# Kernel optimization log

Hardware: AMD Instinct MI355X
Metric: run time of the kernel (lower is better)

Reference implementation:

```python
import jax, jax.numpy as jnp
import numpy as np

B, N_PER, K = 8, 4096, 16          # graphs, nodes per graph, knn neighbors
D_IN, D_H, D_OUT = 32, 64, 128     # feature_nn: 35->64->64, global_nn: 64->128
N = B * N_PER


def setup_inputs() -> dict:
    key = jax.random.key(0)
    ks = jax.random.split(key, 8)
    sc = lambda fan: 1.0 / np.sqrt(fan)
    x = jax.random.normal(ks[0], (N, D_IN), jnp.float32)
    pos = jax.random.normal(ks[1], (N, 3), jnp.float32)
    batch = jnp.repeat(jnp.arange(B, dtype=jnp.int32), N_PER)
    fW1 = jax.random.normal(ks[2], (D_IN + 3, D_H), jnp.float32) * sc(D_IN + 3)
    fb1 = jnp.zeros((D_H,), jnp.float32)
    fW2 = jax.random.normal(ks[3], (D_H, D_H), jnp.float32) * sc(D_H)
    fb2 = jnp.zeros((D_H,), jnp.float32)
    gW = jax.random.normal(ks[4], (D_H, D_OUT), jnp.float32) * sc(D_H)
    gb = jnp.zeros((D_OUT,), jnp.float32)
    return {"x": x, "pos": pos, "batch": batch,
            "fW1": fW1, "fb1": fb1, "fW2": fW2, "fb2": fb2,
            "gW": gW, "gb": gb}


def reference(x, pos, batch, fW1, fb1, fW2, fb2, gW, gb):
    # ---- knn(pos, pos, k, batch, batch): per-graph k nearest (self included) ----
    posb = pos.reshape(B, N_PER, 3)
    sq = jnp.sum(posb * posb, axis=-1)                      # [B, Nper]
    dist = sq[:, :, None] + sq[:, None, :] - 2.0 * jnp.einsum('bnd,bmd->bnm', posb, posb)
    _, nbr = jax.lax.top_k(-dist, K)                        # [B, Nper, K] local neighbor idx
    offs = (jnp.arange(B, dtype=nbr.dtype) * N_PER)[:, None, None]
    col = (nbr + offs).reshape(-1)                          # edge_index[1]: neighbor (x) idx
    row = jnp.repeat(jnp.arange(N, dtype=col.dtype), K)     # edge_index[0]: query (y) idx

    # ---- PointConv: msg = feature_nn(cat[x_j, pos_j - pos_i]), max-aggregate at i ----
    # PyG flow source_to_target: j = edge_index[0] = row (query), i = edge_index[1] = col.
    msg = jnp.concatenate([x[row], pos[row] - pos[col]], axis=1)  # [E, 35]
    h = jax.nn.relu(msg @ fW1 + fb1)
    h = jax.nn.relu(h @ fW2 + fb2)                          # [E, 64]
    agg = jax.ops.segment_max(h, col, num_segments=N)       # max aggregation
    agg = jnp.where(jnp.isfinite(agg), agg, 0.0)            # PyG fills empty segments with 0
    out = jax.nn.relu(agg @ gW + gb)                        # global_nn
    return (out, pos, batch)
```

## Files before the change

kernel.cpp:

```cpp
#include <hip/hip_runtime.h>
#include <hip/hip_bf16.h>

#define N_PER    4096
#define KNBR     16
#define NTOT     32768
#define D_IN     32
#define D_H      64
#define D_OUT    128
#define E_TOT    (NTOT * KNBR)

#define OUT1_OFF (NTOT * D_OUT)
#define OUT2_OFF (NTOT * D_OUT + NTOT*3)

#define KNN_INF 3.4e38f

typedef __attribute__((ext_vector_type(8))) short bf16x8;
typedef __attribute__((ext_vector_type(4))) float f32x4;

__device__ float          g_posf[NTOT * 3];
__device__ float          g_scf[NTOT];
__device__ float4         g_pos4[NTOT];
__device__ int            g_nbr[E_TOT];
__device__ unsigned short g_base1h[NTOT * D_H];
__device__ uint4          g_Bfrag[2 * 4 * 64];
__device__ float          g_Wd[3 * D_H];
__device__ float          g_fb2v[D_H];
__device__ int            g_cnt[NTOT];
__device__ int            g_bsum[NTOT / 256];
__device__ int            g_offs[NTOT + 1];
__device__ int            g_cursor[NTOT];
__device__ int            g_inlist[E_TOT];
__device__ float          g_agg[NTOT * D_H];

__device__ __forceinline__ float ldf(const void* p, int i, int bf) {
    if (bf) return __uint_as_float(((unsigned)((const unsigned short*)p)[i]) << 16);
    return ((const float*)p)[i];
}
__device__ __forceinline__ unsigned bf16rne(float f) {
    unsigned u = __float_as_uint(f);
    return (u + 0x7FFFu + ((u >> 16) & 1u)) >> 16;
}
__device__ __forceinline__ void stf(void* p, int i, float v, int bf) {
    if (bf) ((unsigned short*)p)[i] = (unsigned short)bf16rne(v);
    else    ((float*)p)[i] = v;
}
__device__ __forceinline__ float b2f(unsigned short h) {
    return __uint_as_float(((unsigned)h) << 16);
}
__device__ __forceinline__ int wave_probe(const void* x) {
    unsigned wv = ((const unsigned*)x)[threadIdx.x & 63];
    unsigned e = (wv >> 7) & 0xFFu;
    unsigned long long mk = __ballot(e >= 110u && e <= 140u);
    return (__popcll(mk) >= 32) ? 1 : 0;
}

__global__ __launch_bounds__(256) void prep_kernel(const void* __restrict__ x,
                                                   const void* __restrict__ pos,
                                                   const void* __restrict__ fW1,
                                                   const void* __restrict__ fb1,
                                                   const void* __restrict__ fW2,
                                                   const void* __restrict__ fb2) {
    const int bf = wave_probe(x);
    const int b = blockIdx.x;
    if (b < 1024) {
        const int i0 = b * 256 + threadIdx.x;
        const int stride = 1024 * 256;
        for (int i = i0; i < NTOT * 3; i += stride) g_posf[i] = ldf(pos, i, bf);
        {
#pragma clang fp contract(off)
            for (int i = i0; i < NTOT; i += stride) {
                float a = ldf(pos, i * 3 + 0, bf);
                float c2 = ldf(pos, i * 3 + 1, bf);
                float c3 = ldf(pos, i * 3 + 2, bf);
                float sc = a * a + c2 * c2 + c3 * c3;
                g_scf[i] = sc;
                g_pos4[i] = make_float4(-2.0f * a, -2.0f * c2, -2.0f * c3, sc);
                g_cnt[i] = 0;
            }
        }
        for (int i = i0; i < NTOT * D_H; i += stride) g_agg[i] = 0.0f;
    } else if (b < 2048) {
        int lane = threadIdx.x & 63, wid = threadIdx.x >> 6;
        int n0 = (b - 1024) * 32 + wid * 8;
        float wcol[D_IN];
#pragma unroll
        for (int k = 0; k < D_IN; k++) wcol[k] = ldf(fW1, k * D_H + lane, bf);
        float bb = ldf(fb1, lane, bf);
        if (bf) {
            const unsigned short* xp = (const unsigned short*)x;
            for (int r = 0; r < 8; r++) {
                int n = n0 + r;
                const uint4* xr = (const uint4*)(xp + (size_t)n * D_IN);
                float acc = bb;
#pragma unroll
                for (int q4 = 0; q4 < 4; q4++) {
                    uint4 w4 = xr[q4];
                    unsigned ww[4] = {w4.x, w4.y, w4.z, w4.w};
#pragma unroll
                    for (int p = 0; p < 4; p++) {
                        int k = q4 * 8 + p * 2;
                        acc += __uint_as_float(ww[p] << 16) * wcol[k];
                        acc += __uint_as_float(ww[p] & 0xFFFF0000u) * wcol[k + 1];
                    }
                }
                g_base1h[(size_t)n * D_H + lane] = (unsigned short)bf16rne(acc);
            }
        } else {
            const float* xp = (const float*)x;
            for (int r = 0; r < 8; r++) {
                int n = n0 + r;
                const float4* xr = (const float4*)(xp + (size_t)n * D_IN);
                float acc = bb;
#pragma unroll
                for (int q4 = 0; q4 < 8; q4++) {
                    float4 w4 = xr[q4];
                    int k = q4 * 4;
                    acc += w4.x * wcol[k] + w4.y * wcol[k + 1] + w4.z * wcol[k + 2] + w4.w * wcol[k + 3];
                }
                g_base1h[(size_t)n * D_H + lane] = (unsigned short)bf16rne(acc);
            }
        }
    } else {
        for (int t = threadIdx.x; t < 3 * D_H; t += 256) g_Wd[t] = ldf(fW1, D_IN * D_H + t, bf);
        if (threadIdx.x < D_H) g_fb2v[threadIdx.x] = ldf(fb2, threadIdx.x, bf);
        for (int idx = threadIdx.x; idx < 512; idx += 256) {
            int lane = idx & 63, nt = (idx >> 6) & 3, ks = idx >> 8;
            int n = nt * 16 + (lane & 15);
            int k0 = ks * 32 + ((lane >> 4) << 3);
            unsigned wds[4];
#pragma unroll
            for (int jp = 0; jp < 4; jp++) {
                unsigned lo = bf16rne(ldf(fW2, (k0 + 2 * jp) * D_H + n, bf));
                unsigned hi = bf16rne(ldf(fW2, (k0 + 2 * jp + 1) * D_H + n, bf));
                wds[jp] = lo | (hi << 16);
            }
            g_Bfrag[idx] = make_uint4(wds[0], wds[1], wds[2], wds[3]);
        }
    }
}

__global__ __launch_bounds__(512) void knn_kernel() {
#pragma clang fp contract(off)
    __shared__ float4 s_c4[2048];
    __shared__ int s_i[8][8][64];
    const int lane = threadIdx.x & 63;
    const int wid  = threadIdx.x >> 6;
    const int qbase = blockIdx.x * 64 + wid * 8;
    const int cbase = (qbase >> 12) << 12;
    const float* cp  = g_posf + cbase * 3;
    const float* csc = g_scf + cbase;

    float qx[8], qy[8], qz[8], qs[8];
#pragma unroll
    for (int r = 0; r < 8; r++) {
        qx[r] = g_posf[(qbase + r) * 3 + 0];
        qy[r] = g_posf[(qbase + r) * 3 + 1];
        qz[r] = g_posf[(qbase + r) * 3 + 2];
        qs[r] = g_scf[qbase + r];
    }

    float m[8];
#pragma unroll
    for (int r = 0; r < 8; r++) m[r] = KNN_INF;
    for (int ch = 0; ch < 2; ch++) {
        __syncthreads();
        const float4* gp = g_pos4 + cbase + ch * 2048;
        for (int i = threadIdx.x; i < 2048; i += 512) s_c4[i] = gp[i];
        __syncthreads();
#pragma unroll 4
        for (int c = 0; c < 32; c++) {
            float4 v4 = s_c4[c * 64 + lane];
#pragma unroll
            for (int r = 0; r < 8; r++) {
                float d = fmaf(v4.z, qz[r], fmaf(v4.y, qy[r], fmaf(v4.x, qx[r], v4.w)));
                m[r] = fminf(m[r], d);
            }
        }
    }

    float T[8];
#pragma unroll
    for (int r = 0; r < 8; r++) {
        float v = m[r];
#pragma unroll
        for (int k = 2; k <= 64; k <<= 1) {
#pragma unroll
            for (int j2 = k >> 1; j2 >= 1; j2 >>= 1) {
                float pv = __shfl_xor(v, j2);
                bool keepMin = (((lane & j2) == 0) == ((lane & k) == 0));
                bool tp = ((pv < v) == keepMin);
                v = tp ? pv : v;
            }
        }
        T[r] = __shfl(v, 15) + 1e-3f;
    }

    int cnt[8];
#pragma unroll
    for (int r = 0; r < 8; r++) cnt[r] = 0;
    for (int ch = 0; ch < 2; ch++) {
        __syncthreads();
        const float4* gp = g_pos4 + cbase + ch * 2048;
        for (int i = threadIdx.x; i < 2048; i += 512) s_c4[i] = gp[i];
        __syncthreads();
        for (int c = 0; c < 32; c++) {
            int jj = c * 64 + lane;
            float4 v4 = s_c4[jj];
#pragma unroll
            for (int r = 0; r < 8; r++) {
                float d = fmaf(v4.z, qz[r], fmaf(v4.y, qy[r], fmaf(v4.x, qx[r], v4.w)));
                bool p = (d <= T[r]);
                unsigned long long mk = __ballot(p);
                if (mk) {
                    int pre = (int)__popcll(mk & ((1ull << lane) - 1ull));
                    int slot = cnt[r] + pre;
                    if (p && slot < 64) s_i[wid][r][slot] = cbase + ch * 2048 + jj;
                    cnt[r] += (int)__popcll(mk);
                }
            }
        }
    }

#pragma unroll
    for (int r = 0; r < 8; r++) {
        int q = qbase + r;
        if (cnt[r] <= 64) {
            int S = cnt[r];
            int idx = (lane < S) ? s_i[wid][r][lane] : 0x7FFFFFFF;
            float d = KNN_INF;
            if (lane < S) {
                float px = g_posf[idx * 3], py = g_posf[idx * 3 + 1], pz = g_posf[idx * 3 + 2];
                float sc = g_scf[idx];
                float dot = px * qx[r] + py * qy[r] + pz * qz[r];
                d = (qs[r] + sc) - 2.0f * dot;
            }
#pragma unroll
            for (int k = 2; k <= 64; k <<= 1) {
#pragma unroll
                for (int j2 = k >> 1; j2 >= 1; j2 >>= 1) {
                    float pd = __shfl_xor(d, j2);
                    int   pi = __shfl_xor(idx, j2);
                    bool keepMin = (((lane & j2) == 0) == ((lane & k) == 0));
                    bool lt = (pd < d) || (pd == d && pi < idx);
                    bool tp = (lt == keepMin);
                    d   = tp ? pd : d;
                    idx = tp ? pi : idx;
                }
            }
            if (lane < 16) {
                g_nbr[q * KNBR + lane] = idx;
                atomicAdd(&g_cnt[idx & (NTOT - 1)], 1);
            }
        } else {
            float lastd = -KNN_INF; int lasti = -1;
            for (int t = 0; t < 16; t++) {
                float bd = KNN_INF; int bi = 0x7FFFFFFF;
                for (int c = 0; c < 64; c++) {
                    int jj = c * 64 + lane;
                    float px = cp[jj * 3], py = cp[jj * 3 + 1], pz = cp[jj * 3 + 2];
                    float sc = csc[jj];
                    float dot = px * qx[r] + py * qy[r] + pz * qz[r];
                    float dd = (qs[r] + sc) - 2.0f * dot;
                    int gj = cbase + jj;
                    bool after  = (dd > lastd) || (dd == lastd && gj > lasti);
                    bool better = (dd < bd) || (dd == bd && gj < bi);
                    if (after && better) { bd = dd; bi = gj; }
                }
#pragma unroll
                for (int s2 = 1; s2 < 64; s2 <<= 1) {
                    float od = __shfl_xor(bd, s2);
                    int   oi = __shfl_xor(bi, s2);
                    if (od < bd || (od == bd && oi < bi)) { bd = od; bi = oi; }
                }
                if (lane == 0) {
                    g_nbr[q * KNBR + t] = bi;
                    atomicAdd(&g_cnt[bi & (NTOT - 1)], 1);
                }
                lastd = bd; lasti = bi;
            }
        }
    }
}

__global__ __launch_bounds__(256) void scanA_kernel() {
    __shared__ int red[4];
    int t = threadIdx.x, lane = t & 63, w = t >> 6;
    int v = g_cnt[blockIdx.x * 256 + t];
    int s = v;
#pragma unroll
    for (int off = 1; off < 64; off <<= 1) s += __shfl_xor(s, off);
    if (lane == 0) red[w] = s;
    __syncthreads();
    if (t == 0) g_bsum[blockIdx.x] = red[0] + red[1] + red[2] + red[3];
}

__global__ __launch_bounds__(256) void scanC_kernel() {
    __shared__ int sred[4];
    __shared__ int wsum[4];
    int t = threadIdx.x, lane = t & 63, w = t >> 6;
    int contrib = (t < 128 && t < blockIdx.x) ? g_bsum[t] : 0;
    int rs = contrib;
#pragma unroll
    for (int off = 1; off < 64; off <<= 1) rs += __shfl_xor(rs, off);
    if (lane == 0) sred[w] = rs;
    __syncthreads();
    int base = sred[0] + sred[1] + sred[2] + sred[3];

    int i = blockIdx.x * 256 + t;
    int v = g_cnt[i];
    int inc = v;
#pragma unroll
    for (int off = 1; off < 64; off <<= 1) {
        int u = __shfl_up(inc, off);
        if (lane >= off) inc += u;
    }
    if (lane == 63) wsum[w] = inc;
    __syncthreads();
    int wbase = 0;
    for (int k = 0; k < w; k++) wbase += wsum[k];
    int excl = base + wbase + inc - v;
    g_offs[i] = excl;
    g_cursor[i] = excl;
    if (i == NTOT - 1) g_offs[NTOT] = E_TOT;
}

__global__ void scatter_kernel() {
    int e = blockIdx.x * 256 + threadIdx.x;
    int c = g_nbr[e] & (NTOT - 1);
    int slot = atomicAdd(&g_cursor[c], 1);
    g_inlist[slot & (E_TOT - 1)] = e;
}

__global__ __launch_bounds__(256) void edge_kernel() {
    __shared__ unsigned short sA[256 * 72];
    __shared__ int scol[256];
    const int t    = threadIdx.x;
    const int lane = t & 63;
    const int w    = t >> 6;
    const int slot0 = blockIdx.x * 256;

    {
        int e = g_inlist[slot0 + t];
        int n = (e >> 4) & (NTOT - 1);
        int j = g_nbr[e] & (NTOT - 1);
        scol[t] = j;
        float dx = g_posf[n * 3 + 0] - g_posf[j * 3 + 0];
        float dy = g_posf[n * 3 + 1] - g_posf[j * 3 + 1];
        float dz = g_posf[n * 3 + 2] - g_posf[j * 3 + 2];
        const unsigned short* b1 = g_base1h + (size_t)n * D_H;
#pragma unroll
        for (int d0 = 0; d0 < D_H; d0 += 8) {
            uint4 p = *(const uint4*)(b1 + d0);
            unsigned pw[4] = {p.x, p.y, p.z, p.w};
            unsigned qw[4];
#pragma unroll
            for (int jp = 0; jp < 4; jp++) {
                int d = d0 + 2 * jp;
                float v0 = __uint_as_float(pw[jp] << 16)
                         + dx * g_Wd[d]     + dy * g_Wd[64 + d]     + dz * g_Wd[128 + d];
                float v1 = __uint_as_float(pw[jp] & 0xFFFF0000u)
                         + dx * g_Wd[d + 1] + dy * g_Wd[64 + d + 1] + dz * g_Wd[128 + d + 1];
                v0 = fmaxf(v0, 0.f); v1 = fmaxf(v1, 0.f);
                qw[jp] = bf16rne(v0) | (bf16rne(v1) << 16);
            }
            *(uint4*)(&sA[t * 72 + d0]) = make_uint4(qw[0], qw[1], qw[2], qw[3]);
        }
    }
    __syncthreads();

    f32x4 acc[4][4];
#pragma unroll
    for (int a = 0; a < 4; a++)
#pragma unroll
        for (int b = 0; b < 4; b++) acc[a][b] = (f32x4){0.f, 0.f, 0.f, 0.f};

    const int quad = lane >> 4;
    const int l15  = lane & 15;
#pragma unroll
    for (int ks = 0; ks < 2; ks++) {
        bf16x8 bfrag[4];
#pragma unroll
        for (int nt = 0; nt < 4; nt++)
            bfrag[nt] = ((const bf16x8*)g_Bfrag)[ks * 256 + nt * 64 + lane];
#pragma unroll
        for (int mt = 0; mt < 4; mt++) {
            int row = w * 64 + mt * 16 + l15;
            bf16x8 afrag = *(const bf16x8*)(&sA[row * 72 + ks * 32 + quad * 8]);
#pragma unroll
            for (int nt = 0; nt < 4; nt++)
                acc[mt][nt] = __builtin_amdgcn_mfma_f32_16x16x32_bf16(afrag, bfrag[nt], acc[mt][nt], 0, 0, 0);
        }
    }
    __syncthreads();

#pragma unroll
    for (int nt = 0; nt < 4; nt++) {
        int dim = nt * 16 + l15;
        float bb = g_fb2v[dim];
#pragma unroll
        for (int mt = 0; mt < 4; mt++) {
#pragma unroll
            for (int r = 0; r < 4; r++) {
                int edge = w * 64 + mt * 16 + quad * 4 + r;
                float v = fmaxf(acc[mt][nt][r] + bb, 0.f);
                sA[edge * 72 + dim] = (unsigned short)bf16rne(v);
            }
        }
    }
    __syncthreads();

    {
        const int ls0 = w * 64;
        const int gs0 = slot0 + ls0;
        int cur = -1;
        float vmax = 0.f;
        for (int s = ls0; s < ls0 + 64; s++) {
            int cj = scol[s];
            float v = b2f(sA[s * 72 + lane]);
            if (cj != cur) {
                if (cur >= 0) {
                    int lo = g_offs[cur], hi = g_offs[cur + 1];
                    if (lo >= gs0 && hi <= gs0 + 64)
                        g_agg[(size_t)cur * D_H + lane] = vmax;
                    else
                        atomicMax((unsigned*)&g_agg[(size_t)cur * D_H + lane], __float_as_uint(vmax));
                }
                cur = cj; vmax = v;
            } else {
                vmax = fmaxf(vmax, v);
            }
        }
        if (cur >= 0) {
            int lo = g_offs[cur], hi = g_offs[cur + 1];
            if (lo >= gs0 && hi <= gs0 + 64)
                g_agg[(size_t)cur * D_H + lane] = vmax;
            else
                atomicMax((unsigned*)&g_agg[(size_t)cur * D_H + lane], __float_as_uint(vmax));
        }
    }
}

__global__ __launch_bounds__(256) void outmisc_kernel(const void* __restrict__ x,
                                                      const void* __restrict__ gW,
                                                      const void* __restrict__ gb,
                                                      const int* __restrict__ batch,
                                                      const void* __restrict__ pos,
                                                      void* __restrict__ out) {
    const int bf = wave_probe(x);
    const int b = blockIdx.x;
    if (b < 2048) {
        int t = threadIdx.x, d = t & 127, half = t >> 7;
        float gcol[D_H];
#pragma unroll
        for (int k = 0; k < D_H; k++) gcol[k] = ldf(gW, k * D_OUT + d, bf);
        float bb = ldf(gb, d, bf);
        int n0 = b * 16 + half * 8;
        for (int r = 0; r < 8; r++) {
            int n = n0 + r;
            float acc = bb;
#pragma unroll
            for (int k = 0; k < D_H; k++) acc += g_agg[(size_t)n * D_H + k] * gcol[k];
            stf(out, n * D_OUT + d, fmaxf(acc, 0.f), bf);
        }
    } else {
        int i = (b - 2048) * 256 + threadIdx.x;
        if (bf) {
            if (i < NTOT * 3) ((unsigned short*)out)[OUT1_OFF + i] = ((const unsigned short*)pos)[i];
            if (i < NTOT)     ((unsigned short*)out)[OUT2_OFF + i] = (unsigned short)bf16rne((float)batch[i]);
        } else {
            if (i < NTOT * 3) ((float*)out)[OUT1_OFF + i] = ((const float*)pos)[i];
            if (i < NTOT)     ((float*)out)[OUT2_OFF + i] = (float)batch[i];
        }
    }
}

extern "C" void kernel_launch(void* const* d_in, const int* in_sizes, int n_in,
                              void* d_out, int out_size, void* d_ws, size_t ws_size,
                              hipStream_t stream) {
    const void* x     = d_in[0];
    const void* pos   = d_in[1];
    const int*  batch = (const int*)d_in[2];
    const void* fW1   = d_in[3];
    const void* fb1   = d_in[4];
    const void* fW2   = d_in[5];
    const void* fb2   = d_in[6];
    const void* gW    = d_in[7];
    const void* gb    = d_in[8];

    hipLaunchKernelGGL(prep_kernel,    dim3(2049),        dim3(256), 0, stream, x, pos, fW1, fb1, fW2, fb2);
    hipLaunchKernelGGL(knn_kernel,     dim3(NTOT / 64),   dim3(512), 0, stream);
    hipLaunchKernelGGL(scanA_kernel,   dim3(NTOT / 256),  dim3(256), 0, stream);
    hipLaunchKernelGGL(scanC_kernel,   dim3(NTOT / 256),  dim3(256), 0, stream);
    hipLaunchKernelGGL(scatter_kernel, dim3(E_TOT / 256), dim3(256), 0, stream);
    hipLaunchKernelGGL(edge_kernel,    dim3(E_TOT / 256), dim3(256), 0, stream);
    hipLaunchKernelGGL(outmisc_kernel, dim3(2048 + (NTOT * 3 + 255) / 256), dim3(256), 0, stream,
                       x, gW, gb, batch, pos, d_out);
}
```

Measured before the change: 270.7 us.

## Compute KNN threshold pass with bf16 MFMA and split candidate columns across waves

Replaces the scalar FMA first pass of the KNN threshold search with bf16 MFMA tiles. Each wave covers a slice of the candidates for all 64 queries in the block, and the per-column minima are combined through shared memory. Because bf16 rounding makes the estimated distances inaccurate, a dtype-dependent margin widens the threshold. A second ballot count checks that at least 16 candidates fall safely inside it, otherwise the existing fallback path runs. This trades extra candidates and an added ballot per row in the second pass for a much cheaper first pass.

```diff
diff --git a/kernel.cpp b/kernel.cpp
--- a/kernel.cpp
+++ b/kernel.cpp
@@ -16,10 +16,13 @@
 
 typedef __attribute__((ext_vector_type(8))) short bf16x8;
 typedef __attribute__((ext_vector_type(4))) float f32x4;
-
+union U16 { uint4 u; bf16x8 v; };
+
+__device__ int            g_dtflag;
 __device__ float          g_posf[NTOT * 3];
 __device__ float          g_scf[NTOT];
 __device__ float4         g_pos4[NTOT];
+__device__ uint4          g_nbB[NTOT];
 __device__ int            g_nbr[E_TOT];
 __device__ unsigned short g_base1h[NTOT * D_H];
 __device__ uint4          g_Bfrag[2 * 4 * 64];
@@ -75,6 +78,13 @@
                 float sc = a * a + c2 * c2 + c3 * c3;
                 g_scf[i] = sc;
                 g_pos4[i] = make_float4(-2.0f * a, -2.0f * c2, -2.0f * c3, sc);
+                unsigned xh = bf16rne(-2.0f * a);
+                unsigned yh = bf16rne(-2.0f * c2);
+                unsigned zh = bf16rne(-2.0f * c3);
+                unsigned sh = bf16rne(sc);
+                float slo = sc - b2f((unsigned short)sh);
+                unsigned sl = bf16rne(slo);
+                g_nbB[i] = make_uint4(xh | (yh << 16), zh | (sh << 16), sl, 0u);
                 g_cnt[i] = 0;
             }
         }
@@ -121,6 +131,7 @@
             }
         }
     } else {
+        if (threadIdx.x == 0) g_dtflag = bf;
         for (int t = threadIdx.x; t < 3 * D_H; t += 256) g_Wd[t] = ldf(fW1, D_IN * D_H + t, bf);
         if (threadIdx.x < D_H) g_fb2v[threadIdx.x] = ldf(fb2, threadIdx.x, bf);
         for (int idx = threadIdx.x; idx < 512; idx += 256) {
@@ -141,14 +152,20 @@
 
 __global__ __launch_bounds__(512) void knn_kernel() {
 #pragma clang fp contract(off)
-    __shared__ float4 s_c4[2048];
+    __shared__ __align__(16) float s_part[8192];
     __shared__ int s_i[8][8][64];
+    float4* s_c4 = (float4*)s_part;
     const int lane = threadIdx.x & 63;
     const int wid  = threadIdx.x >> 6;
-    const int qbase = blockIdx.x * 64 + wid * 8;
-    const int cbase = (qbase >> 12) << 12;
+    const int quad = lane >> 4;
+    const int l15  = lane & 15;
+    const int qblk  = blockIdx.x * 64;
+    const int qbase = qblk + wid * 8;
+    const int cbase = (qblk >> 12) << 12;
     const float* cp  = g_posf + cbase * 3;
     const float* csc = g_scf + cbase;
+    const float margin = g_dtflag ? 2e-3f : 0.05f;
+    const float gap = 1e-4f;
 
     float qx[8], qy[8], qz[8], qs[8];
 #pragma unroll
@@ -159,29 +176,59 @@
         qs[r] = g_scf[qbase + r];
     }
 
-    float m[8];
-#pragma unroll
-    for (int r = 0; r < 8; r++) m[r] = KNN_INF;
-    for (int ch = 0; ch < 2; ch++) {
-        __syncthreads();
-        const float4* gp = g_pos4 + cbase + ch * 2048;
-        for (int i = threadIdx.x; i < 2048; i += 512) s_c4[i] = gp[i];
-        __syncthreads();
-#pragma unroll 4
-        for (int c = 0; c < 32; c++) {
-            float4 v4 = s_c4[c * 64 + lane];
-#pragma unroll
-            for (int r = 0; r < 8; r++) {
-                float d = fmaf(v4.z, qz[r], fmaf(v4.y, qy[r], fmaf(v4.x, qx[r], v4.w)));
-                m[r] = fminf(m[r], d);
-            }
-        }
-    }
+    bf16x8 afrag[4];
+#pragma unroll
+    for (int mt = 0; mt < 4; mt++) {
+        int q = qblk + mt * 16 + l15;
+        unsigned w0 = bf16rne(g_posf[q * 3 + 0]) | (bf16rne(g_posf[q * 3 + 1]) << 16);
+        unsigned w1 = bf16rne(g_posf[q * 3 + 2]) | (0x3F80u << 16);
+        unsigned w2 = 0x3F80u;
+        U16 uu;
+        uu.u = make_uint4(quad == 0 ? w0 : 0u, quad == 0 ? w1 : 0u,
+                          quad == 0 ? w2 : 0u, 0u);
+        afrag[mt] = uu.v;
+    }
+    f32x4 mrow[4];
+#pragma unroll
+    for (int mt = 0; mt < 4; mt++) mrow[mt] = (f32x4){KNN_INF, KNN_INF, KNN_INF, KNN_INF};
+    {
+        const uint4* nb = g_nbB + cbase + wid * 512;
+        const f32x4 zero = (f32x4){0.f, 0.f, 0.f, 0.f};
+#pragma unroll 2
+        for (int t = 0; t < 32; t++) {
+            uint4 v = nb[t * 16 + l15];
+            U16 ub;
+            ub.u = make_uint4(quad == 0 ? v.x : 0u, quad == 0 ? v.y : 0u,
+                              quad == 0 ? v.z : 0u, 0u);
+            bf16x8 bfrag = ub.v;
+            f32x4 d0 = __builtin_amdgcn_mfma_f32_16x16x32_bf16(afrag[0], bfrag, zero, 0, 0, 0);
+            f32x4 d1 = __builtin_amdgcn_mfma_f32_16x16x32_bf16(afrag[1], bfrag, zero, 0, 0, 0);
+            f32x4 d2 = __builtin_amdgcn_mfma_f32_16x16x32_bf16(afrag[2], bfrag, zero, 0, 0, 0);
+            f32x4 d3 = __builtin_amdgcn_mfma_f32_16x16x32_bf16(afrag[3], bfrag, zero, 0, 0, 0);
+#pragma unroll
+            for (int i = 0; i < 4; i++) {
+                mrow[0][i] = fminf(mrow[0][i], d0[i]);
+                mrow[1][i] = fminf(mrow[1][i], d1[i]);
+                mrow[2][i] = fminf(mrow[2][i], d2[i]);
+                mrow[3][i] = fminf(mrow[3][i], d3[i]);
+            }
+        }
+    }
+#pragma unroll
+    for (int mt = 0; mt < 4; mt++) {
+#pragma unroll
+        for (int r = 0; r < 4; r++) {
+            int q = mt * 16 + quad * 4 + r;
+            s_part[q * 128 + wid * 16 + l15] = mrow[mt][r];
+        }
+    }
+    __syncthreads();
 
     float T[8];
 #pragma unroll
     for (int r = 0; r < 8; r++) {
-        float v = m[r];
+        int q = wid * 8 + r;
+        float v = fminf(s_part[q * 128 + lane], s_part[q * 128 + 64 + lane]);
 #pragma unroll
         for (int k = 2; k <= 64; k <<= 1) {
 #pragma unroll
@@ -192,12 +239,12 @@
                 v = tp ? pv : v;
             }
         }
-        T[r] = __shfl(v, 15) + 1e-3f;
-    }
-
-    int cnt[8];
-#pragma unroll
-    for (int r = 0; r < 8; r++) cnt[r] = 0;
+        T[r] = __shfl(v, 15) + margin;
+    }
+
+    int cnt[8], cnts[8];
+#pragma unroll
+    for (int r = 0; r < 8; r++) { cnt[r] = 0; cnts[r] = 0; }
     for (int ch = 0; ch < 2; ch++) {
         __syncthreads();
         const float4* gp = g_pos4 + cbase + ch * 2048;
@@ -216,6 +263,7 @@
                     int slot = cnt[r] + pre;
                     if (p && slot < 64) s_i[wid][r][slot] = cbase + ch * 2048 + jj;
                     cnt[r] += (int)__popcll(mk);
+                    cnts[r] += (int)__popcll(__ballot(d <= T[r] - gap));
                 }
             }
         }
@@ -224,7 +272,7 @@
 #pragma unroll
     for (int r = 0; r < 8; r++) {
         int q = qbase + r;
-        if (cnt[r] <= 64) {
+        if (cnt[r] <= 64 && cnts[r] >= 16) {
             int S = cnt[r];
             int idx = (lane < S) ? s_i[wid][r][lane] : 0x7FFFFFFF;
             float d = KNN_INF;
```

New measurement: 481.6 us. +77.9%, slower.

## Use MFMA for global_nn GEMM and shared-atomic candidate collection in kNN

Applied to the files above, without the earlier changes.

The global_nn output layer is moved onto bf16 MFMA 16x16x32 instructions when inputs are bf16. gW is pre-packed into B fragments in the prep kernel, and each 256-thread block handles 256 nodes from a padded LDS tile. Separately, the kNN candidate collection replaces per-row ballot/popcount bookkeeping with LDS atomicAdd slot allocation. This lowers the scalar FMA work in the output GEMM and the ballot overhead in kNN. The trade-offs are that candidate order becomes nondeterministic and the fp32 output path now runs fewer, longer blocks.

```diff
diff --git a/kernel.cpp b/kernel.cpp
--- a/kernel.cpp
+++ b/kernel.cpp
@@ -23,8 +23,10 @@
 __device__ int            g_nbr[E_TOT];
 __device__ unsigned short g_base1h[NTOT * D_H];
 __device__ uint4          g_Bfrag[2 * 4 * 64];
+__device__ uint4          g_gBfrag[2 * 8 * 64];
 __device__ float          g_Wd[3 * D_H];
 __device__ float          g_fb2v[D_H];
+__device__ float          g_gbf[D_OUT];
 __device__ int            g_cnt[NTOT];
 __device__ int            g_bsum[NTOT / 256];
 __device__ int            g_offs[NTOT + 1];
@@ -59,7 +61,9 @@
                                                    const void* __restrict__ fW1,
                                                    const void* __restrict__ fb1,
                                                    const void* __restrict__ fW2,
-                                                   const void* __restrict__ fb2) {
+                                                   const void* __restrict__ fb2,
+                                                   const void* __restrict__ gW,
+                                                   const void* __restrict__ gb) {
     const int bf = wave_probe(x);
     const int b = blockIdx.x;
     if (b < 1024) {
@@ -123,6 +127,7 @@
     } else {
         for (int t = threadIdx.x; t < 3 * D_H; t += 256) g_Wd[t] = ldf(fW1, D_IN * D_H + t, bf);
         if (threadIdx.x < D_H) g_fb2v[threadIdx.x] = ldf(fb2, threadIdx.x, bf);
+        if (threadIdx.x < D_OUT) g_gbf[threadIdx.x] = ldf(gb, threadIdx.x, bf);
         for (int idx = threadIdx.x; idx < 512; idx += 256) {
             int lane = idx & 63, nt = (idx >> 6) & 3, ks = idx >> 8;
             int n = nt * 16 + (lane & 15);
@@ -136,6 +141,19 @@
             }
             g_Bfrag[idx] = make_uint4(wds[0], wds[1], wds[2], wds[3]);
         }
+        for (int idx = threadIdx.x; idx < 1024; idx += 256) {
+            int lane = idx & 63, nt = (idx >> 6) & 7, ks = idx >> 9;
+            int n = nt * 16 + (lane & 15);
+            int k0 = ks * 32 + ((lane >> 4) << 3);
+            unsigned wds[4];
+#pragma unroll
+            for (int jp = 0; jp < 4; jp++) {
+                unsigned lo = bf16rne(ldf(gW, (k0 + 2 * jp) * D_OUT + n, bf));
+                unsigned hi = bf16rne(ldf(gW, (k0 + 2 * jp + 1) * D_OUT + n, bf));
+                wds[jp] = lo | (hi << 16);
+            }
+            g_gBfrag[idx] = make_uint4(wds[0], wds[1], wds[2], wds[3]);
+        }
     }
 }
 
@@ -143,6 +161,7 @@
 #pragma clang fp contract(off)
     __shared__ float4 s_c4[2048];
     __shared__ int s_i[8][8][64];
+    __shared__ int s_cnt[8][8];
     const int lane = threadIdx.x & 63;
     const int wid  = threadIdx.x >> 6;
     const int qbase = blockIdx.x * 64 + wid * 8;
@@ -195,9 +214,7 @@
         T[r] = __shfl(v, 15) + 1e-3f;
     }
 
-    int cnt[8];
-#pragma unroll
-    for (int r = 0; r < 8; r++) cnt[r] = 0;
+    if (lane < 8) s_cnt[wid][lane] = 0;
     for (int ch = 0; ch < 2; ch++) {
         __syncthreads();
         const float4* gp = g_pos4 + cbase + ch * 2048;
@@ -206,16 +223,13 @@
         for (int c = 0; c < 32; c++) {
             int jj = c * 64 + lane;
             float4 v4 = s_c4[jj];
+            int gidx = cbase + ch * 2048 + jj;
 #pragma unroll
             for (int r = 0; r < 8; r++) {
                 float d = fmaf(v4.z, qz[r], fmaf(v4.y, qy[r], fmaf(v4.x, qx[r], v4.w)));
-                bool p = (d <= T[r]);
-                unsigned long long mk = __ballot(p);
-                if (mk) {
-                    int pre = (int)__popcll(mk & ((1ull << lane) - 1ull));
-                    int slot = cnt[r] + pre;
-                    if (p && slot < 64) s_i[wid][r][slot] = cbase + ch * 2048 + jj;
-                    cnt[r] += (int)__popcll(mk);
+                if (d <= T[r]) {
+                    int slot = atomicAdd(&s_cnt[wid][r], 1);
+                    if (slot < 64) s_i[wid][r][slot] = gidx;
                 }
             }
         }
@@ -224,8 +238,9 @@
 #pragma unroll
     for (int r = 0; r < 8; r++) {
         int q = qbase + r;
-        if (cnt[r] <= 64) {
-            int S = cnt[r];
+        int cnt = s_cnt[wid][r];
+        if (cnt <= 64) {
+            int S = cnt;
             int idx = (lane < S) ? s_i[wid][r][lane] : 0x7FFFFFFF;
             float d = KNN_INF;
             if (lane < S) {
@@ -442,28 +457,83 @@
 
 __global__ __launch_bounds__(256) void outmisc_kernel(const void* __restrict__ x,
                                                       const void* __restrict__ gW,
-                                                      const void* __restrict__ gb,
                                                       const int* __restrict__ batch,
                                                       const void* __restrict__ pos,
                                                       void* __restrict__ out) {
     const int bf = wave_probe(x);
     const int b = blockIdx.x;
-    if (b < 2048) {
-        int t = threadIdx.x, d = t & 127, half = t >> 7;
-        float gcol[D_H];
-#pragma unroll
-        for (int k = 0; k < D_H; k++) gcol[k] = ldf(gW, k * D_OUT + d, bf);
-        float bb = ldf(gb, d, bf);
-        int n0 = b * 16 + half * 8;
-        for (int r = 0; r < 8; r++) {
-            int n = n0 + r;
-            float acc = bb;
-#pragma unroll
-            for (int k = 0; k < D_H; k++) acc += g_agg[(size_t)n * D_H + k] * gcol[k];
-            stf(out, n * D_OUT + d, fmaxf(acc, 0.f), bf);
+    if (b < 128) {
+        const int t = threadIdx.x;
+        const int lane = t & 63;
+        const int w = t >> 6;
+        const int n0 = b * 256;
+        if (bf) {
+            __shared__ unsigned short sA[256 * 72];
+            {
+                const float4* ar = (const float4*)(g_agg + (size_t)(n0 + t) * D_H);
+#pragma unroll
+                for (int d0 = 0; d0 < D_H; d0 += 8) {
+                    float4 p0 = ar[d0 / 4], p1 = ar[d0 / 4 + 1];
+                    unsigned q0 = bf16rne(p0.x) | (bf16rne(p0.y) << 16);
+                    unsigned q1 = bf16rne(p0.z) | (bf16rne(p0.w) << 16);
+                    unsigned q2 = bf16rne(p1.x) | (bf16rne(p1.y) << 16);
+                    unsigned q3 = bf16rne(p1.z) | (bf16rne(p1.w) << 16);
+                    *(uint4*)(&sA[t * 72 + d0]) = make_uint4(q0, q1, q2, q3);
+                }
+            }
+            __syncthreads();
+            const int quad = lane >> 4;
+            const int l15  = lane & 15;
+            bf16x8 afrag[4][2];
+#pragma unroll
+            for (int mt = 0; mt < 4; mt++) {
+                int row = w * 64 + mt * 16 + l15;
+#pragma unroll
+                for (int ks = 0; ks < 2; ks++)
+                    afrag[mt][ks] = *(const bf16x8*)(&sA[row * 72 + ks * 32 + quad * 8]);
+            }
+            unsigned short* outh = (unsigned short*)out;
+#pragma unroll
+            for (int nt = 0; nt < 8; nt++) {
+                f32x4 acc[4];
+#pragma unroll
+                for (int mt = 0; mt < 4; mt++) acc[mt] = (f32x4){0.f, 0.f, 0.f, 0.f};
+#pragma unroll
+                for (int ks = 0; ks < 2; ks++) {
+                    bf16x8 bfrag = ((const bf16x8*)g_gBfrag)[ks * 512 + nt * 64 + lane];
+#pragma unroll
+                    for (int mt = 0; mt < 4; mt++)
+                        acc[mt] = __builtin_amdgcn_mfma_f32_16x16x32_bf16(afrag[mt][ks], bfrag, acc[mt], 0, 0, 0);
+                }
+                int dim = nt * 16 + l15;
+                float bb = g_gbf[dim];
+#pragma unroll
+                for (int mt = 0; mt < 4; mt++) {
+#pragma unroll
+                    for (int r = 0; r < 4; r++) {
+                        int n = n0 + w * 64 + mt * 16 + quad * 4 + r;
+                        float v = fmaxf(acc[mt][r] + bb, 0.f);
+                        outh[n * D_OUT + dim] = (unsigned short)bf16rne(v);
+                    }
+                }
+            }
+        } else {
+            int d = t & 127, half = t >> 7;
+            float gcol[D_H];
+#pragma unroll
+            for (int k = 0; k < D_H; k++) gcol[k] = ldf(gW, k * D_OUT + d, 0);
+            float bb = g_gbf[d];
+            int r0 = n0 + half * 128;
+            for (int r = 0; r < 128; r++) {
+                int n = r0 + r;
+                float acc = bb;
+#pragma unroll
+                for (int k = 0; k < D_H; k++) acc += g_agg[(size_t)n * D_H + k] * gcol[k];
+                ((float*)out)[n * D_OUT + d] = fmaxf(acc, 0.f);
+            }
         }
     } else {
-        int i = (b - 2048) * 256 + threadIdx.x;
+        int i = (b - 128) * 256 + threadIdx.x;
         if (bf) {
             if (i < NTOT * 3) ((unsigned short*)out)[OUT1_OFF + i] = ((const unsigned short*)pos)[i];
             if (i < NTOT)     ((unsigned short*)out)[OUT2_OFF + i] = (unsigned short)bf16rne((float)batch[i]);
@@ -487,12 +557,12 @@
     const void* gW    = d_in[7];
     const void* gb    = d_in[8];
 
-    hipLaunchKernelGGL(prep_kernel,    dim3(2049),        dim3(256), 0, stream, x, pos, fW1, fb1, fW2, fb2);
+    hipLaunchKernelGGL(prep_kernel,    dim3(2049),        dim3(256), 0, stream, x, pos, fW1, fb1, fW2, fb2, gW, gb);
     hipLaunchKernelGGL(knn_kernel,     dim3(NTOT / 64),   dim3(512), 0, stream);
     hipLaunchKernelGGL(scanA_kernel,   dim3(NTOT / 256),  dim3(256), 0, stream);
     hipLaunchKernelGGL(scanC_kernel,   dim3(NTOT / 256),  dim3(256), 0, stream);
     hipLaunchKernelGGL(scatter_kernel, dim3(E_TOT / 256), dim3(256), 0, stream);
     hipLaunchKernelGGL(edge_kernel,    dim3(E_TOT / 256), dim3(256), 0, stream);
-    hipLaunchKernelGGL(outmisc_kernel, dim3(2048 + (NTOT * 3 + 255) / 256), dim3(256), 0, stream,
-                       x, gW, gb, batch, pos, d_out);
-}
+    hipLaunchKernelGGL(outmisc_kernel, dim3(128 + (NTOT * 3 + 255) / 256), dim3(256), 0, stream,
+                       x, gW, batch, pos, d_out);
+}
```

Result: slower. 353.4 us (+30.6%).
